# Optimization experiments

Measured on AMD Instinct MI355X. Metric: run time of the kernel, lower is better.

The kernel has to match this reference:

```python
import jax, jax.numpy as jnp
import numpy as np

SIGMA = 1.0
EPS = 1e-8
LN2 = float(np.log(2.0))


def setup_inputs() -> dict:
    key = jax.random.key(0)
    k1, k2, k3 = jax.random.split(key, 3)
    B, D = 2048, 128
    scores = jax.random.normal(k1, (B, D), dtype=jnp.float32)
    relevances = jax.random.randint(k2, (B, D), 0, 5, dtype=jnp.int32)
    query_lengths = jax.random.randint(k3, (B,), 1, D + 1, dtype=jnp.int32)
    return {"scores": scores, "relevances": relevances, "query_lengths": query_lengths}


def reference(scores, relevances, query_lengths):
    # scores: [B, D] float, relevances: [B, D] int grades, query_lengths: [B] int
    B, D = scores.shape
    doc_mask = jnp.arange(D)[None, :] < query_lengths[:, None]          # [B, D]
    pair_mask = doc_mask[:, :, None] & doc_mask[:, None, :]             # [B, D, D]

    gains = jnp.where(doc_mask, jnp.exp2(relevances.astype(scores.dtype)) - 1.0, 0.0)  # 2^y - 1

    # pairwise score diffs and gain deltas, zeroed on padding
    diff = scores[:, :, None] - scores[:, None, :]                      # [B, D, D]
    delta = jnp.where(pair_mask, jnp.abs(gains[:, :, None] - gains[:, None, :]), 0.0)

    # ideal DCG: gains sorted descending within each query's valid prefix
    sort_key = jnp.where(doc_mask, gains, -jnp.inf)
    sorted_gains = -jnp.sort(-sort_key, axis=1)                         # descending
    ranks = jnp.arange(D, dtype=scores.dtype)
    discount = 1.0 / jnp.log2(ranks + 2.0)                              # [D]
    rank_mask = jnp.arange(D)[None, :] < query_lengths[:, None]
    ideal_dcg = jnp.sum(jnp.where(rank_mask, sorted_gains * discount[None, :], 0.0), axis=1)  # [B]

    # log2(sigmoid(sigma * diff)) == log_sigmoid(sigma*diff) / ln(2)
    log2_prob = jax.nn.log_sigmoid(SIGMA * diff) / LN2                  # [B, D, D]
    num = jnp.sum(delta * log2_prob, axis=(1, 2))                       # [B]

    per_query = -num / (ideal_dcg + EPS)
    return jnp.sum(per_query) / B
```

## Files before the change

kernel.cpp:

```cpp
#include <hip/hip_runtime.h>

#define SIGMA  1.0f
#define LOG2E  1.4426950408889634f
#define EPSF   1e-8f

#define EXP2F(x) __builtin_amdgcn_exp2f(x)
#define LOG2F(x) __builtin_amdgcn_logf(x)

__global__ __launch_bounds__(256) void ndcg_loss_kernel(
    const float* __restrict__ scores,
    const int*   __restrict__ relevances,
    const int*   __restrict__ qlen,
    float*       __restrict__ out,
    float invB)
{
    __shared__ float s_sc[128];
    __shared__ float s_g[128];
    __shared__ int   s_cnt[5];
    __shared__ float s_red[4][2];

    const int b   = blockIdx.x;
    const int tid = threadIdx.x;
    const int L   = qlen[b];

    if (tid < 5) s_cnt[tid] = 0;
    __syncthreads();

    if (tid < 128) {
        float sc = scores[b * 128 + tid];
        int   r  = relevances[b * 128 + tid];
        r = min(max(r, 0), 4);
        s_sc[tid] = sc;
        bool valid = (tid < L);
        s_g[tid] = valid ? (float)((1 << r) - 1) : 0.0f;
        if (valid) atomicAdd(&s_cnt[r], 1);
    }
    __syncthreads();

    float num = 0.0f;
    {
        const int j  = tid & 127;
        const int r0 = tid >> 7;
        if (j < L) {
            const float sj = s_sc[j];
            const float gj = s_g[j];
            for (int i = r0; i < L; i += 2) {
                float d  = s_sc[i] - sj;
                float dg = fabsf(s_g[i] - gj);
                float y  = d * (SIGMA * LOG2E);
                float lp = fminf(y, 0.0f) - LOG2F(1.0f + EXP2F(-fabsf(y)));
                num += dg * lp;
            }
        }
    }

    float idcg = 0.0f;
    if (tid < 128 && tid < L) {
        int c4 = s_cnt[4], c3 = s_cnt[3], c2 = s_cnt[2], c1 = s_cnt[1];
        int t1 = c4, t2 = t1 + c3, t3 = t2 + c2, t4 = t3 + c1;
        float g = (tid < t1) ? 15.0f :
                  (tid < t2) ?  7.0f :
                  (tid < t3) ?  3.0f :
                  (tid < t4) ?  1.0f : 0.0f;
        idcg = g / LOG2F((float)(tid + 2));
    }

    #pragma unroll
    for (int o = 32; o > 0; o >>= 1) {
        num  += __shfl_down(num,  o, 64);
        idcg += __shfl_down(idcg, o, 64);
    }
    const int w = tid >> 6;
    if ((tid & 63) == 0) { s_red[w][0] = num; s_red[w][1] = idcg; }
    __syncthreads();

    if (tid == 0) {
        float n = s_red[0][0] + s_red[1][0] + s_red[2][0] + s_red[3][0];
        float d = s_red[0][1] + s_red[1][1] + s_red[2][1] + s_red[3][1];
        float per_query = -n / (d + EPSF);
        atomicAdd(out, per_query * invB);
    }
}

extern "C" void kernel_launch(void* const* d_in, const int* in_sizes, int n_in,
                              void* d_out, int out_size, void* d_ws, size_t ws_size,
                              hipStream_t stream)
{
    const float* scores     = (const float*)d_in[0];
    const int*   relevances = (const int*)  d_in[1];
    const int*   qlen       = (const int*)  d_in[2];
    float*       out        = (float*)d_out;

    const int B = in_sizes[2];
    (void)hipMemsetAsync(out, 0, sizeof(float) * out_size, stream);
    ndcg_loss_kernel<<<B, 256, 0, stream>>>(scores, relevances, qlen, out,
                                            1.0f / (float)B);
}
```

Baseline: 86.89 us.

## Exploit pairwise symmetry to halve log-sigmoid evaluations via circular pair enumeration

```diff
diff --git a/kernel.cpp b/kernel.cpp
--- a/kernel.cpp
+++ b/kernel.cpp
@@ -14,10 +14,9 @@
     float*       __restrict__ out,
     float invB)
 {
-    __shared__ float s_sc[128];
-    __shared__ float s_g[128];
-    __shared__ int   s_cnt[5];
-    __shared__ float s_red[4][2];
+    __shared__ float2 s_sg[256];
+    __shared__ int    s_cnt[5];
+    __shared__ float  s_red[4][2];
 
     const int b   = blockIdx.x;
     const int tid = threadIdx.x;
@@ -30,27 +29,33 @@
         float sc = scores[b * 128 + tid];
         int   r  = relevances[b * 128 + tid];
         r = min(max(r, 0), 4);
-        s_sc[tid] = sc;
         bool valid = (tid < L);
-        s_g[tid] = valid ? (float)((1 << r) - 1) : 0.0f;
+        float2 v = make_float2(sc, valid ? (float)((1 << r) - 1) : 0.0f);
+        s_sg[tid] = v;
+        if (tid < L) s_sg[tid + L] = v;
         if (valid) atomicAdd(&s_cnt[r], 1);
     }
     __syncthreads();
 
-    float num = 0.0f;
-    {
-        const int j  = tid & 127;
-        const int r0 = tid >> 7;
-        if (j < L) {
-            const float sj = s_sc[j];
-            const float gj = s_g[j];
-            for (int i = r0; i < L; i += 2) {
-                float d  = s_sc[i] - sj;
-                float dg = fabsf(s_g[i] - gj);
-                float y  = d * (SIGMA * LOG2E);
-                float lp = fminf(y, 0.0f) - LOG2F(1.0f + EXP2F(-fabsf(y)));
-                num += dg * lp;
-            }
+    float acc = 0.0f;
+    const int j  = tid & 127;
+    const int ph = tid >> 7;
+    if (j < L) {
+        const float sj = s_sg[j].x;
+        const float gj = s_sg[j].y;
+        const int Kfull = (L - 1) >> 1;
+        #pragma unroll 4
+        for (int k = 1 + ph; k <= Kfull; k += 2) {
+            const float2 v = s_sg[j + k];
+            float a = fabsf(v.x - sj) * (SIGMA * LOG2E);
+            float u = LOG2F(1.0f + EXP2F(-a));
+            acc = fmaf(fabsf(v.y - gj), fmaf(2.0f, u, a), acc);
+        }
+        if (((L & 1) == 0) && ph == 0 && j < (L >> 1)) {
+            const float2 v = s_sg[j + (L >> 1)];
+            float a = fabsf(v.x - sj) * (SIGMA * LOG2E);
+            float u = LOG2F(1.0f + EXP2F(-a));
+            acc = fmaf(fabsf(v.y - gj), fmaf(2.0f, u, a), acc);
         }
     }
 
@@ -67,18 +72,17 @@
 
     #pragma unroll
     for (int o = 32; o > 0; o >>= 1) {
-        num  += __shfl_down(num,  o, 64);
+        acc  += __shfl_down(acc,  o, 64);
         idcg += __shfl_down(idcg, o, 64);
     }
     const int w = tid >> 6;
-    if ((tid & 63) == 0) { s_red[w][0] = num; s_red[w][1] = idcg; }
+    if ((tid & 63) == 0) { s_red[w][0] = acc; s_red[w][1] = idcg; }
     __syncthreads();
 
     if (tid == 0) {
         float n = s_red[0][0] + s_red[1][0] + s_red[2][0] + s_red[3][0];
         float d = s_red[0][1] + s_red[1][1] + s_red[2][1] + s_red[3][1];
-        float per_query = -n / (d + EPSF);
-        atomicAdd(out, per_query * invB);
+        atomicAdd(out, (n / (d + EPSF)) * invB);
     }
 }
 
```

After: 85.68 us. About the same (-1.4%).
